# Kernel tuning notes

Measured on AMD Instinct MI355X. Metric: run time of the kernel, lower is better.

The kernel has to match this reference:

```python
import jax, jax.numpy as jnp
import numpy as np

S, D = 8192, 2048      # sequence length, feature dim (input_size)
H, E, K, L = 64, 64, 2, 64  # gate hidden, expert count, top-k, expert layer_size
EPS = 1e-12            # torch F.normalize eps


def setup_inputs() -> dict:
    key = jax.random.key(0)
    ks = jax.random.split(key, 5)
    x = jax.random.normal(ks[0], (S, D), dtype=jnp.float32)
    # torch nn.Linear weights have shape [out_features, in_features]
    Wg_in = jax.random.normal(ks[1], (H, D), dtype=jnp.float32) * 0.02   # gate.input
    Wg_lin = jax.random.normal(ks[2], (E, H), dtype=jnp.float32) * 0.02  # gate.linear
    Wg_out = jax.random.normal(ks[3], (1, S), dtype=jnp.float32) * 0.02  # gate.output
    We = jax.random.normal(ks[4], (E, L, D), dtype=jnp.float32) * 0.02   # expert weight bank
    return {"x": x, "Wg_in": Wg_in, "Wg_lin": Wg_lin, "Wg_out": Wg_out, "We": We}


def reference(x, Wg_in, Wg_lin, Wg_out, We):
    # --- SparseGate (eval mode: dropout = identity) ---
    h = x @ Wg_in.T                         # [S, H]
    logits = h @ Wg_lin.T                   # [S, E]
    scores = (logits.T @ Wg_out.T)[:, 0]    # Linear(S,1) applied to [E,S] -> [E]
    topv, idx = jax.lax.top_k(scores, K)    # global top-k experts for whole input
    g = jax.nn.softmax(topv)                # softmax over the k selected logits

    # --- dispatch to k selected experts (FFNN: Linear -> normalize(-1) -> GELU) ---
    Wsel = We[idx]                          # [K, L, D]
    z = jnp.einsum('sd,kld->ksl', x, Wsel)  # [K, S, L]
    z = z / jnp.maximum(jnp.linalg.norm(z, axis=-1, keepdims=True), EPS)
    z = jax.nn.gelu(z, approximate=False)   # torch GELU default is exact erf

    # --- weighted combine: sum_k g_k * expert_k(x) ---
    return jnp.einsum('k,ksl->sl', g, z)    # [S, L]
```

## Files before the change

### kernel.cpp

```cpp
#include <hip/hip_runtime.h>
#include <hip/hip_bf16.h>
#include <math.h>

#define D_DIM 2048
#define L_DIM 64
#define E_NUM 64
#define H_DIM 64

typedef float f32x4_t __attribute__((ext_vector_type(4)));
typedef __bf16 bf16x8_t __attribute__((ext_vector_type(8)));

#define WS_UPART 0u
#define WS_U     (512u * 2048u * 4u)
#define WS_V     (WS_U + 2048u * 4u)
#define WS_META  (WS_V + 256u)
#define WS_WB    (WS_META + 64u)
#define WS_XB    (WS_WB + 128u * 2048u * 2u)
#define WS_PART  (WS_XB + 8192u * 2048u * 2u)


__global__ void k_upart(const float* __restrict__ x, const float* __restrict__ wout,
                        float* __restrict__ upart, __hip_bfloat16* __restrict__ xbt) {
  const int t = threadIdx.x;
  const int d8 = t * 8;
  const int s0 = blockIdx.x * 16;
  const int kstep = d8 >> 6;
  const int kc = (d8 >> 3) & 7;
  float a0 = 0.f, a1 = 0.f, a2 = 0.f, a3 = 0.f;
  float a4 = 0.f, a5 = 0.f, a6 = 0.f, a7 = 0.f;
  for (int i = 0; i < 16; ++i) {
    const int row = s0 + i;
    const float w = wout[row];
    const float4 pa = *reinterpret_cast<const float4*>(x + (size_t)row * D_DIM + d8);
    const float4 pb = *reinterpret_cast<const float4*>(x + (size_t)row * D_DIM + d8 + 4);
    a0 += pa.x * w; a1 += pa.y * w; a2 += pa.z * w; a3 += pa.w * w;
    a4 += pb.x * w; a5 += pb.y * w; a6 += pb.z * w; a7 += pb.w * w;
    union { __hip_bfloat16 h[8]; uint4 u; } pk;
    pk.h[0] = __float2bfloat16(pa.x); pk.h[1] = __float2bfloat16(pa.y);
    pk.h[2] = __float2bfloat16(pa.z); pk.h[3] = __float2bfloat16(pa.w);
    pk.h[4] = __float2bfloat16(pb.x); pk.h[5] = __float2bfloat16(pb.y);
    pk.h[6] = __float2bfloat16(pb.z); pk.h[7] = __float2bfloat16(pb.w);
    const int mt = row >> 7, rl = row & 127;
    const size_t off = (size_t)mt * 262144 + kstep * 8192 + rl * 64 +
                       ((kc ^ (rl & 7)) * 8);
    *reinterpret_cast<uint4*>(xbt + off) = pk.u;
  }
  float* up = upart + (size_t)blockIdx.x * D_DIM + d8;
  *reinterpret_cast<float4*>(up)     = make_float4(a0, a1, a2, a3);
  *reinterpret_cast<float4*>(up + 4) = make_float4(a4, a5, a6, a7);
}

__global__ void k_ufinish(const float* __restrict__ upart, float* __restrict__ u) {
  const int d = blockIdx.x * 256 + threadIdx.x;
  float s = 0.f;
#pragma unroll 8
  for (int c = 0; c < 512; ++c) s += upart[(size_t)c * D_DIM + d];
  u[d] = s;
}

__global__ void k_v(const float* __restrict__ wg_in, const float* __restrict__ u,
                    float* __restrict__ v) {
  const int h = blockIdx.x;
  const int t = threadIdx.x;
  const float4* wr = reinterpret_cast<const float4*>(wg_in + (size_t)h * D_DIM);
  const float4* ur = reinterpret_cast<const float4*>(u);
  float s = 0.f;
#pragma unroll
  for (int i = t; i < 512; i += 256) {
    const float4 a = wr[i];
    const float4 b = ur[i];
    s += a.x * b.x + a.y * b.y + a.z * b.z + a.w * b.w;
  }
  __shared__ float red[4];
#pragma unroll
  for (int off = 32; off; off >>= 1) s += __shfl_down(s, off, 64);
  if ((t & 63) == 0) red[t >> 6] = s;
  __syncthreads();
  if (t == 0) v[h] = red[0] + red[1] + red[2] + red[3];
}

__global__ void k_gate(const float* __restrict__ wg_lin, const float* __restrict__ v,
                       int* __restrict__ sel, float* __restrict__ g) {
  __shared__ float vv[H_DIM];
  __shared__ float sc[E_NUM];
  const int t = threadIdx.x;
  vv[t] = v[t];
  __syncthreads();
  float s = 0.f;
#pragma unroll 8
  for (int hh = 0; hh < H_DIM; ++hh) s += wg_lin[t * H_DIM + hh] * vv[hh];
  sc[t] = s;
  __syncthreads();
  if (t == 0) {
    int b1 = 0; float m1 = sc[0];
    for (int e = 1; e < E_NUM; ++e) { if (sc[e] > m1) { m1 = sc[e]; b1 = e; } }
    int b2 = -1; float m2 = -3.4e38f;
    for (int e = 0; e < E_NUM; ++e) {
      if (e != b1 && sc[e] > m2) { m2 = sc[e]; b2 = e; }
    }
    const float e2 = expf(m2 - m1);
    const float g0 = 1.0f / (1.0f + e2);
    sel[0] = b1; sel[1] = b2;
    g[0] = g0; g[1] = 1.0f - g0;
  }
}

__global__ void k_wb(const float* __restrict__ we, const int* __restrict__ sel,
                     __hip_bfloat16* __restrict__ wbt) {
  const int n = blockIdx.x;
  const int e = sel[n >> 6];
  const int l = n & 63;
  const float* src = we + ((size_t)e * L_DIM + l) * D_DIM;
  const int t = threadIdx.x;
  const int d8 = t * 8;
  const int kstep = d8 >> 6;
  const int kc = (d8 >> 3) & 7;
  const float4 a = reinterpret_cast<const float4*>(src)[2 * t];
  const float4 b = reinterpret_cast<const float4*>(src)[2 * t + 1];
  union { __hip_bfloat16 h[8]; uint4 u; } pk;
  pk.h[0] = __float2bfloat16(a.x); pk.h[1] = __float2bfloat16(a.y);
  pk.h[2] = __float2bfloat16(a.z); pk.h[3] = __float2bfloat16(a.w);
  pk.h[4] = __float2bfloat16(b.x); pk.h[5] = __float2bfloat16(b.y);
  pk.h[6] = __float2bfloat16(b.z); pk.h[7] = __float2bfloat16(b.w);
  const size_t off = (size_t)kstep * 8192 + n * 64 + ((kc ^ (n & 7)) * 8);
  *reinterpret_cast<uint4*>(wbt + off) = pk.u;
}

__device__ __forceinline__ void async_ld16(const void* gp, void* lp) {
  __builtin_amdgcn_global_load_lds(
      (const __attribute__((address_space(1))) unsigned int*)gp,
      (__attribute__((address_space(3))) unsigned int*)lp, 16, 0, 0);
}

__device__ __forceinline__ float gelu_f(float v) {
  return 0.5f * v * (1.0f + erff(v * 0.70710678118654752440f));
}

__global__ __launch_bounds__(256, 4) void k_moe_gemm(
    const __hip_bfloat16* __restrict__ xbt, const __hip_bfloat16* __restrict__ wbt,
    float* __restrict__ part) {
  __shared__ __align__(16) unsigned char lds[24576];

  const int tid = threadIdx.x;
  const int w = tid >> 6, lane = tid & 63;
  const int wm = w >> 1, wn = w & 1;
  const int mb = blockIdx.x;
  const int kg = blockIdx.y;
  const int fr = lane & 15, fq = lane >> 4;

  unsigned char* ldsA = lds;
  unsigned char* ldsB = lds + 8192;

  const size_t abase = (size_t)(mb >> 1) * 262144 + (size_t)(mb & 1) * 4096;

  f32x4_t acc[2][4];
#pragma unroll
  for (int mf = 0; mf < 2; ++mf)
#pragma unroll
    for (int nf = 0; nf < 4; ++nf) acc[mf][nf] = (f32x4_t){0.f, 0.f, 0.f, 0.f};

  for (int kk = 0; kk < 4; ++kk) {
    const size_t tbase = (size_t)(kg * 4 + kk) * 8192;
    if (kk) __syncthreads();
#pragma unroll
    for (int ph = 0; ph < 2; ++ph) {
      const int c = ph * 256 + tid;
      async_ld16(xbt + abase + tbase + c * 8, ldsA + c * 16);
    }
#pragma unroll
    for (int ph = 0; ph < 4; ++ph) {
      const int c = ph * 256 + tid;
      async_ld16(wbt + tbase + c * 8, ldsB + c * 16);
    }
    __syncthreads();
    union fragu { uint4 u; bf16x8_t v; };
    fragu af[2][2], bf_[4][2];
#pragma unroll
    for (int mf = 0; mf < 2; ++mf)
#pragma unroll
      for (int ks = 0; ks < 2; ++ks) {
        const int ar = wm * 32 + mf * 16 + fr;
        const int kq = ks * 4 + fq;
        af[mf][ks].u = *reinterpret_cast<const uint4*>(
            ldsA + ar * 128 + ((kq ^ (ar & 7)) * 16));
      }
#pragma unroll
    for (int nf = 0; nf < 4; ++nf)
#pragma unroll
      for (int ks = 0; ks < 2; ++ks) {
        const int br = wn * 64 + nf * 16 + fr;
        const int kq = ks * 4 + fq;
        bf_[nf][ks].u = *reinterpret_cast<const uint4*>(
            ldsB + br * 128 + ((kq ^ (br & 7)) * 16));
      }
#pragma unroll
    for (int mf = 0; mf < 2; ++mf)
#pragma unroll
      for (int nf = 0; nf < 4; ++nf) {
        acc[mf][nf] = __builtin_amdgcn_mfma_f32_16x16x32_bf16(
            af[mf][0].v, bf_[nf][0].v, acc[mf][nf], 0, 0, 0);
        acc[mf][nf] = __builtin_amdgcn_mfma_f32_16x16x32_bf16(
            af[mf][1].v, bf_[nf][1].v, acc[mf][nf], 0, 0, 0);
      }
  }

#pragma unroll
  for (int mf = 0; mf < 2; ++mf)
#pragma unroll
    for (int nf = 0; nf < 4; ++nf)
#pragma unroll
      for (int reg = 0; reg < 4; ++reg) {
        const int r = mb * 64 + wm * 32 + mf * 16 + fq * 4 + reg;
        const int c = wn * 64 + nf * 16 + fr;
        part[((size_t)kg * 8192 + r) * 128 + c] = acc[mf][nf][reg];
      }
}

__global__ __launch_bounds__(256) void k_finish(const float* __restrict__ part,
                                                const float* __restrict__ gw,
                                                float* __restrict__ out) {
  __shared__ float z[32 * 132];
  __shared__ float ps[32 * 8];
  const int tid = threadIdx.x;
  const int m0 = blockIdx.x * 32;
  const float g0 = gw[0], g1 = gw[1];
  const size_t KSTRIDE = (size_t)8192 * 128;
#pragma unroll
  for (int p = 0; p < 4; ++p) {
    const int idx = p * 256 + tid;
    const int r = idx >> 5, c4 = (idx & 31) * 4;
    const float* pp = part + ((size_t)(m0 + r)) * 128 + c4;
    f32x4_t s = (f32x4_t){0.f, 0.f, 0.f, 0.f};
#pragma unroll
    for (int kgi = 0; kgi < 8; ++kgi)
      s = s + *reinterpret_cast<const f32x4_t*>(pp + kgi * KSTRIDE);
    z[r * 132 + c4 + 0] = s[0];
    z[r * 132 + c4 + 1] = s[1];
    z[r * 132 + c4 + 2] = s[2];
    z[r * 132 + c4 + 3] = s[3];
  }
  __syncthreads();
  {
    const int r = tid >> 3, seg = tid & 7;
    float s = 0.f;
#pragma unroll
    for (int i2 = 0; i2 < 16; ++i2) {
      const float t2 = z[r * 132 + seg * 16 + i2];
      s += t2 * t2;
    }
    ps[r * 8 + seg] = s;
  }
  __syncthreads();
  {
    const int r = tid >> 3, j = tid & 7;
    const float s0 = ps[r * 8 + 0] + ps[r * 8 + 1] + ps[r * 8 + 2] + ps[r * 8 + 3];
    const float s1 = ps[r * 8 + 4] + ps[r * 8 + 5] + ps[r * 8 + 6] + ps[r * 8 + 7];
    const float i0 = 1.0f / fmaxf(sqrtf(s0), 1e-12f);
    const float i1 = 1.0f / fmaxf(sqrtf(s1), 1e-12f);
    float o[8];
#pragma unroll
    for (int i2 = 0; i2 < 8; ++i2) {
      const int c = j * 8 + i2;
      const float za = z[r * 132 + c] * i0;
      const float zb2 = z[r * 132 + 64 + c] * i1;
      o[i2] = g0 * gelu_f(za) + g1 * gelu_f(zb2);
    }
    float4* op = reinterpret_cast<float4*>(out + (size_t)(m0 + r) * 64 + j * 8);
    op[0] = make_float4(o[0], o[1], o[2], o[3]);
    op[1] = make_float4(o[4], o[5], o[6], o[7]);
  }
}

extern "C" void kernel_launch(void* const* d_in, const int* in_sizes, int n_in,
                              void* d_out, int out_size, void* d_ws, size_t ws_size,
                              hipStream_t stream) {
  (void)in_sizes; (void)n_in; (void)out_size; (void)ws_size;
  const float* x      = (const float*)d_in[0];
  const float* wg_in  = (const float*)d_in[1];
  const float* wg_lin = (const float*)d_in[2];
  const float* wg_out = (const float*)d_in[3];
  const float* we     = (const float*)d_in[4];
  float* out = (float*)d_out;
  char* ws = (char*)d_ws;

  float* upart = (float*)(ws + WS_UPART);
  float* u     = (float*)(ws + WS_U);
  float* v     = (float*)(ws + WS_V);
  int*   sel   = (int*)(ws + WS_META);
  float* g     = (float*)(ws + WS_META + 8);
  __hip_bfloat16* wbt = (__hip_bfloat16*)(ws + WS_WB);
  __hip_bfloat16* xbt = (__hip_bfloat16*)(ws + WS_XB);
  float* part = (float*)(ws + WS_PART);

  k_upart  <<<512, 256, 0, stream>>>(x, wg_out, upart, xbt);
  k_ufinish<<<8, 256, 0, stream>>>(upart, u);
  k_v      <<<64, 256, 0, stream>>>(wg_in, u, v);
  k_gate   <<<1, 64, 0, stream>>>(wg_lin, v, sel, g);
  k_wb     <<<128, 256, 0, stream>>>(we, sel, wbt);
  k_moe_gemm<<<dim3(128, 8), 256, 0, stream>>>(xbt, wbt, part);
  k_finish <<<256, 256, 0, stream>>>(part, g, out);
}
```

Baseline: 185.0 us.

## Convert x to bf16 inside GEMM instead of staging a bf16 copy

Removes the bf16 swizzled copy of x written by the gate reduction kernel. The GEMM now loads fp32 x directly, converts it to bf16 in registers and stores it to a padded LDS tile with a 144-byte row stride, replacing the XOR swizzle. The gate partial-sum kernel is reshaped to 64-row chunks on a 2x128 grid, which cuts the partial count to 128. This avoids writing and re-reading 32MB of bf16 data. In exchange the GEMM reads twice as many bytes of x per tile, and its A loads become synchronous instead of async-to-LDS.

```diff
diff --git a/kernel.cpp b/kernel.cpp
--- a/kernel.cpp
+++ b/kernel.cpp
@@ -11,50 +11,33 @@
 typedef __bf16 bf16x8_t __attribute__((ext_vector_type(8)));
 
 #define WS_UPART 0u
-#define WS_U     (512u * 2048u * 4u)
+#define WS_U     (128u * 2048u * 4u)
 #define WS_V     (WS_U + 2048u * 4u)
 #define WS_META  (WS_V + 256u)
 #define WS_WB    (WS_META + 64u)
-#define WS_XB    (WS_WB + 128u * 2048u * 2u)
-#define WS_PART  (WS_XB + 8192u * 2048u * 2u)
+#define WS_PART  (WS_WB + 128u * 2048u * 2u)
 
 
 __global__ void k_upart(const float* __restrict__ x, const float* __restrict__ wout,
-                        float* __restrict__ upart, __hip_bfloat16* __restrict__ xbt) {
-  const int t = threadIdx.x;
-  const int d8 = t * 8;
-  const int s0 = blockIdx.x * 16;
-  const int kstep = d8 >> 6;
-  const int kc = (d8 >> 3) & 7;
-  float a0 = 0.f, a1 = 0.f, a2 = 0.f, a3 = 0.f;
-  float a4 = 0.f, a5 = 0.f, a6 = 0.f, a7 = 0.f;
-  for (int i = 0; i < 16; ++i) {
-    const int row = s0 + i;
-    const float w = wout[row];
-    const float4 pa = *reinterpret_cast<const float4*>(x + (size_t)row * D_DIM + d8);
-    const float4 pb = *reinterpret_cast<const float4*>(x + (size_t)row * D_DIM + d8 + 4);
-    a0 += pa.x * w; a1 += pa.y * w; a2 += pa.z * w; a3 += pa.w * w;
-    a4 += pb.x * w; a5 += pb.y * w; a6 += pb.z * w; a7 += pb.w * w;
-    union { __hip_bfloat16 h[8]; uint4 u; } pk;
-    pk.h[0] = __float2bfloat16(pa.x); pk.h[1] = __float2bfloat16(pa.y);
-    pk.h[2] = __float2bfloat16(pa.z); pk.h[3] = __float2bfloat16(pa.w);
-    pk.h[4] = __float2bfloat16(pb.x); pk.h[5] = __float2bfloat16(pb.y);
-    pk.h[6] = __float2bfloat16(pb.z); pk.h[7] = __float2bfloat16(pb.w);
-    const int mt = row >> 7, rl = row & 127;
-    const size_t off = (size_t)mt * 262144 + kstep * 8192 + rl * 64 +
-                       ((kc ^ (rl & 7)) * 8);
-    *reinterpret_cast<uint4*>(xbt + off) = pk.u;
-  }
-  float* up = upart + (size_t)blockIdx.x * D_DIM + d8;
-  *reinterpret_cast<float4*>(up)     = make_float4(a0, a1, a2, a3);
-  *reinterpret_cast<float4*>(up + 4) = make_float4(a4, a5, a6, a7);
+                        float* __restrict__ upart) {
+  const int d4 = (blockIdx.x * 256 + threadIdx.x) * 4;
+  const int s0 = blockIdx.y * 64;
+  const float* xp = x + (size_t)s0 * D_DIM + d4;
+  float4 acc = make_float4(0.f, 0.f, 0.f, 0.f);
+#pragma unroll 8
+  for (int i = 0; i < 64; ++i) {
+    const float w = wout[s0 + i];
+    const float4 xv = *reinterpret_cast<const float4*>(xp + (size_t)i * D_DIM);
+    acc.x += xv.x * w; acc.y += xv.y * w; acc.z += xv.z * w; acc.w += xv.w * w;
+  }
+  *reinterpret_cast<float4*>(upart + (size_t)blockIdx.y * D_DIM + d4) = acc;
 }
 
 __global__ void k_ufinish(const float* __restrict__ upart, float* __restrict__ u) {
   const int d = blockIdx.x * 256 + threadIdx.x;
   float s = 0.f;
 #pragma unroll 8
-  for (int c = 0; c < 512; ++c) s += upart[(size_t)c * D_DIM + d];
+  for (int c = 0; c < 128; ++c) s += upart[(size_t)c * D_DIM + d];
   u[d] = s;
 }
 
@@ -137,9 +120,11 @@
 }
 
 __global__ __launch_bounds__(256, 4) void k_moe_gemm(
-    const __hip_bfloat16* __restrict__ xbt, const __hip_bfloat16* __restrict__ wbt,
+    const float* __restrict__ x, const __hip_bfloat16* __restrict__ wbt,
     float* __restrict__ part) {
-  __shared__ __align__(16) unsigned char lds[24576];
+  __shared__ __align__(16) unsigned char lds[64 * 144 + 16384];
+  unsigned char* ldsA = lds;
+  unsigned char* ldsB = lds + 64 * 144;
 
   const int tid = threadIdx.x;
   const int w = tid >> 6, lane = tid & 63;
@@ -147,11 +132,7 @@
   const int mb = blockIdx.x;
   const int kg = blockIdx.y;
   const int fr = lane & 15, fq = lane >> 4;
-
-  unsigned char* ldsA = lds;
-  unsigned char* ldsB = lds + 8192;
-
-  const size_t abase = (size_t)(mb >> 1) * 262144 + (size_t)(mb & 1) * 4096;
+  const int m0 = mb * 64;
 
   f32x4_t acc[2][4];
 #pragma unroll
@@ -160,17 +141,27 @@
     for (int nf = 0; nf < 4; ++nf) acc[mf][nf] = (f32x4_t){0.f, 0.f, 0.f, 0.f};
 
   for (int kk = 0; kk < 4; ++kk) {
-    const size_t tbase = (size_t)(kg * 4 + kk) * 8192;
+    const int kstep = kg * 4 + kk;
+    const int k0 = kstep * 64;
     if (kk) __syncthreads();
+#pragma unroll
+    for (int ph = 0; ph < 4; ++ph) {
+      const int c = ph * 256 + tid;
+      async_ld16(wbt + (size_t)kstep * 8192 + c * 8, ldsB + c * 16);
+    }
 #pragma unroll
     for (int ph = 0; ph < 2; ++ph) {
       const int c = ph * 256 + tid;
-      async_ld16(xbt + abase + tbase + c * 8, ldsA + c * 16);
-    }
-#pragma unroll
-    for (int ph = 0; ph < 4; ++ph) {
-      const int c = ph * 256 + tid;
-      async_ld16(wbt + tbase + c * 8, ldsB + c * 16);
+      const int r = c >> 3, c8 = (c & 7) * 8;
+      const float* gp = x + (size_t)(m0 + r) * D_DIM + k0 + c8;
+      const float4 a0 = *reinterpret_cast<const float4*>(gp);
+      const float4 a1 = *reinterpret_cast<const float4*>(gp + 4);
+      union { __hip_bfloat16 h[8]; uint4 u; } pk;
+      pk.h[0] = __float2bfloat16(a0.x); pk.h[1] = __float2bfloat16(a0.y);
+      pk.h[2] = __float2bfloat16(a0.z); pk.h[3] = __float2bfloat16(a0.w);
+      pk.h[4] = __float2bfloat16(a1.x); pk.h[5] = __float2bfloat16(a1.y);
+      pk.h[6] = __float2bfloat16(a1.z); pk.h[7] = __float2bfloat16(a1.w);
+      *reinterpret_cast<uint4*>(ldsA + r * 144 + c8 * 2) = pk.u;
     }
     __syncthreads();
     union fragu { uint4 u; bf16x8_t v; };
@@ -180,9 +171,8 @@
 #pragma unroll
       for (int ks = 0; ks < 2; ++ks) {
         const int ar = wm * 32 + mf * 16 + fr;
-        const int kq = ks * 4 + fq;
         af[mf][ks].u = *reinterpret_cast<const uint4*>(
-            ldsA + ar * 128 + ((kq ^ (ar & 7)) * 16));
+            ldsA + ar * 144 + (ks * 4 + fq) * 16);
       }
 #pragma unroll
     for (int nf = 0; nf < 4; ++nf)
@@ -210,7 +200,7 @@
     for (int nf = 0; nf < 4; ++nf)
 #pragma unroll
       for (int reg = 0; reg < 4; ++reg) {
-        const int r = mb * 64 + wm * 32 + mf * 16 + fq * 4 + reg;
+        const int r = m0 + wm * 32 + mf * 16 + fq * 4 + reg;
         const int c = wn * 64 + nf * 16 + fr;
         part[((size_t)kg * 8192 + r) * 128 + c] = acc[mf][nf][reg];
       }
@@ -289,14 +279,13 @@
   int*   sel   = (int*)(ws + WS_META);
   float* g     = (float*)(ws + WS_META + 8);
   __hip_bfloat16* wbt = (__hip_bfloat16*)(ws + WS_WB);
-  __hip_bfloat16* xbt = (__hip_bfloat16*)(ws + WS_XB);
   float* part = (float*)(ws + WS_PART);
 
-  k_upart  <<<512, 256, 0, stream>>>(x, wg_out, upart, xbt);
+  k_upart  <<<dim3(2, 128), 256, 0, stream>>>(x, wg_out, upart);
   k_ufinish<<<8, 256, 0, stream>>>(upart, u);
   k_v      <<<64, 256, 0, stream>>>(wg_in, u, v);
   k_gate   <<<1, 64, 0, stream>>>(wg_lin, v, sel, g);
   k_wb     <<<128, 256, 0, stream>>>(we, sel, wbt);
-  k_moe_gemm<<<dim3(128, 8), 256, 0, stream>>>(xbt, wbt, part);
+  k_moe_gemm<<<dim3(128, 8), 256, 0, stream>>>(x, wbt, part);
   k_finish <<<256, 256, 0, stream>>>(part, g, out);
 }
```

Result: faster. 160.4 us (-13.3%).
